# Kernel tuning notes

Hardware: AMD Instinct MI355X
Metric: run time of the kernel (lower is better)

The kernel has to match this reference:

```python
import jax, jax.numpy as jnp
import numpy as np

N = 50000
E = 800000
F_IN = 256
HID = 64
HEADS = 4
CLASSES = 8
NEG_SLOPE = 0.2  # PyG GATConv default


def setup_inputs() -> dict:
    key = jax.random.key(0)
    ks = jax.random.split(key, 10)
    x = jax.random.normal(ks[0], (N, F_IN), jnp.float32)
    edge_index = jax.random.randint(ks[1], (2, E), 0, N, dtype=jnp.int32)
    # layer 1: feature -> hidden, heads=4, concat
    W1 = jax.random.normal(ks[2], (F_IN, HEADS * HID), jnp.float32) / np.sqrt(F_IN).astype(np.float32)
    att1_src = jax.random.normal(ks[3], (HEADS, HID), jnp.float32) / np.sqrt(HID).astype(np.float32)
    att1_dst = jax.random.normal(ks[4], (HEADS, HID), jnp.float32) / np.sqrt(HID).astype(np.float32)
    b1 = jnp.zeros((HEADS * HID,), jnp.float32)
    # layer 2: hidden*heads -> classes, heads=1
    W2 = jax.random.normal(ks[5], (HEADS * HID, CLASSES), jnp.float32) / np.sqrt(HEADS * HID).astype(np.float32)
    att2_src = jax.random.normal(ks[6], (1, CLASSES), jnp.float32) / np.sqrt(CLASSES).astype(np.float32)
    att2_dst = jax.random.normal(ks[7], (1, CLASSES), jnp.float32) / np.sqrt(CLASSES).astype(np.float32)
    b2 = jnp.zeros((CLASSES,), jnp.float32)
    return {"x": x, "edge_index": edge_index, "W1": W1, "att1_src": att1_src,
            "att1_dst": att1_dst, "b1": b1, "W2": W2, "att2_src": att2_src,
            "att2_dst": att2_dst, "b2": b2}


def _gat_conv(x, W, a_src, a_dst, b, src, dst, heads, ch, n):
    # h: [N, H, C] per-head projected features
    h = (x @ W).reshape(n, heads, ch)
    alpha_src = jnp.einsum('nhc,hc->nh', h, a_src)  # [N, H]
    alpha_dst = jnp.einsum('nhc,hc->nh', h, a_dst)  # [N, H]
    # per-edge attention logits (gather along edges)
    e = jax.nn.leaky_relu(alpha_src[src] + alpha_dst[dst], NEG_SLOPE)  # [E, H]
    # segment softmax over edges sharing a destination node
    e_max = jax.ops.segment_max(e, dst, num_segments=n)  # [N, H]
    ex = jnp.exp(e - e_max[dst])
    denom = jax.ops.segment_sum(ex, dst, num_segments=n)  # [N, H]
    alpha = ex / denom[dst]  # self-loops guarantee denom > 0
    # weighted scatter-sum of source messages
    out = jax.ops.segment_sum(alpha[..., None] * h[src], dst, num_segments=n)  # [N, H, C]
    return out.reshape(n, heads * ch) + b


def reference(x, edge_index, W1, att1_src, att1_dst, b1, W2, att2_src, att2_dst, b2):
    n = x.shape[0]
    # PyG GATConv adds self-loops by default
    loop = jnp.arange(n, dtype=edge_index.dtype)
    src = jnp.concatenate([edge_index[0], loop])
    dst = jnp.concatenate([edge_index[1], loop])
    h = _gat_conv(x, W1, att1_src, att1_dst, b1, src, dst, HEADS, HID, n)
    h = jax.nn.relu(h)
    # dropout is identity in eval mode (training=self.training)
    out = _gat_conv(h, W2, att2_src, att2_dst, b2, src, dst, 1, CLASSES, n)
    return jax.nn.log_softmax(out, axis=1)
```

## Files before the change

kernel.cpp:

```cpp
#include <hip/hip_runtime.h>
#include <math.h>

#define NNODES 50000
#define NEDGES 800000
#define ETOT   850000
#define SLOPE  0.2f
#define BSLOTS 96
#define CPAD   16
#define NTILE  782
#define BBLK   518

typedef unsigned short ushort_t;
typedef unsigned int   uint_t;
typedef unsigned char  uchar_t;
typedef __attribute__((ext_vector_type(8))) __bf16 bf16x8;
typedef __attribute__((ext_vector_type(4))) float  floatx4;
typedef __attribute__((ext_vector_type(2))) float  floatx2;

#if defined(__has_builtin)
#if __has_builtin(__builtin_amdgcn_cvt_pk_f32_fp8) && __has_builtin(__builtin_amdgcn_cvt_pk_fp8_f32)
#define HWFP8 1
#endif
#endif

__device__ __forceinline__ float leaky(float v) { return fmaxf(v, SLOPE * v); }

__device__ __forceinline__ ushort_t f2bf(float f) {
    uint_t u = __float_as_uint(f);
    uint_t r = (u + 0x7fffu + ((u >> 16) & 1u)) >> 16;
    return (ushort_t)r;
}

__device__ __forceinline__ uint_t f2fp8_sw(float f) {
    uint_t u = __float_as_uint(f);
    uint_t s = (u >> 24) & 0x80u;
    u &= 0x7fffffffu;
    u = u + 0x7ffffu + ((u >> 20) & 1u);
    int e8 = (int)(u >> 23) - 120;
    uint_t m3 = (u >> 20) & 7u;
    if (e8 <= 0) return s;
    if (e8 >= 16) return s | 0x7eu;
    return s | ((uint_t)e8 << 3) | m3;
}
__device__ __forceinline__ float fp8tof_sw(uint_t b) {
    uint_t t = (b & 0x7fu) << 4;
    uint_t r = ((b & 0x80u) << 8) | (t + 0x3C00u);
    return (t >= 0x80u) ? __uint_as_float(r << 16) : 0.f;
}

__device__ __forceinline__ uint_t pk4fp8(float a, float b, float c, float d) {
#ifdef HWFP8
    int pk = 0;
    pk = __builtin_amdgcn_cvt_pk_fp8_f32(a, b, pk, false);
    pk = __builtin_amdgcn_cvt_pk_fp8_f32(c, d, pk, true);
    return (uint_t)pk;
#else
    return f2fp8_sw(a) | (f2fp8_sw(b) << 8) | (f2fp8_sw(c) << 16) | (f2fp8_sw(d) << 24);
#endif
}

__device__ __forceinline__ void dec8acc(uint2 v, float w, float* acc) {
#ifdef HWFP8
    floatx2 f0 = __builtin_amdgcn_cvt_pk_f32_fp8((int)v.x, false);
    floatx2 f1 = __builtin_amdgcn_cvt_pk_f32_fp8((int)v.x, true);
    floatx2 f2 = __builtin_amdgcn_cvt_pk_f32_fp8((int)v.y, false);
    floatx2 f3 = __builtin_amdgcn_cvt_pk_f32_fp8((int)v.y, true);
    acc[0] += w * f0.x; acc[1] += w * f0.y;
    acc[2] += w * f1.x; acc[3] += w * f1.y;
    acc[4] += w * f2.x; acc[5] += w * f2.y;
    acc[6] += w * f3.x; acc[7] += w * f3.y;
#else
    acc[0] += w * fp8tof_sw(v.x & 0xffu);
    acc[1] += w * fp8tof_sw((v.x >> 8) & 0xffu);
    acc[2] += w * fp8tof_sw((v.x >> 16) & 0xffu);
    acc[3] += w * fp8tof_sw(v.x >> 24);
    acc[4] += w * fp8tof_sw(v.y & 0xffu);
    acc[5] += w * fp8tof_sw((v.y >> 8) & 0xffu);
    acc[6] += w * fp8tof_sw((v.y >> 16) & 0xffu);
    acc[7] += w * fp8tof_sw(v.y >> 24);
#endif
}

__device__ __forceinline__ float hsel(float4 v, int h) {
    float t0 = (h & 1) ? v.y : v.x;
    float t1 = (h & 1) ? v.w : v.z;
    return (h & 2) ? t1 : t0;
}

__device__ __forceinline__ int esrc(const int* ei, int e) { return e < NEDGES ? ei[e]          : e - NEDGES; }
__device__ __forceinline__ int edst(const int* ei, int e) { return e < NEDGES ? ei[NEDGES + e] : e - NEDGES; }

__global__ void prep_k(const float* __restrict__ W1, ushort_t* __restrict__ W1c,
                       const float* __restrict__ b1, const float* __restrict__ W2,
                       float* __restrict__ b1p, float* __restrict__ W2p,
                       int* __restrict__ cnt) {
    int bid = blockIdx.x, tid = threadIdx.x;
    int gtid = bid * 256 + tid;
    if (bid < 256) {
        int k = gtid >> 8, n = gtid & 255;
        W1c[(k >> 5) * 8192 + n * 32 + (k & 31)] = f2bf(W1[gtid]);
    } else if (bid == 256) {
        int chp = tid;
        int q = chp & 63, cc = q >> 2, t = q & 3;
        int ch = (chp & 192) | (t * 16 + cc);
        b1p[chp] = b1[ch];
        #pragma unroll
        for (int j = 0; j < 8; ++j) W2p[chp * 8 + j] = W2[ch * 8 + j];
    }
    for (int i = gtid; i < NNODES * CPAD; i += 257 * 256) cnt[i] = 0;
}

__global__ __launch_bounds__(256) void gb_k(const float* __restrict__ X,
                                            const ushort_t* __restrict__ W1c,
                                            const float* __restrict__ att_s,
                                            const float* __restrict__ att_d,
                                            uchar_t* __restrict__ h1f,
                                            float* __restrict__ as1,
                                            float* __restrict__ ad1,
                                            const int* __restrict__ ei,
                                            int* __restrict__ cnt,
                                            int* __restrict__ bkt) {
    __shared__ ushort_t Als[64 * 40];
    __shared__ ushort_t Bls[256 * 40];
    int tid = threadIdx.x;

    if (blockIdx.x >= NTILE) {
        for (int e = (blockIdx.x - NTILE) * 256 + tid; e < ETOT; e += BBLK * 256) {
            int d = edst(ei, e), s = esrc(ei, e);
            int pos = atomicAdd(&cnt[d * CPAD], 1);
            if (pos < BSLOTS) bkt[d * BSLOTS + pos] = s;
        }
        return;
    }

    int row0 = blockIdx.x * 64;
    int wv = tid >> 6, lane = tid & 63, c15 = lane & 15, quad = lane >> 4;
    floatx4 acc[4][4] = {};

    for (int kc = 0; kc < 8; ++kc) {
        __syncthreads();
        {
            int r = tid >> 3, c4 = tid & 7;
            #pragma unroll
            for (int p = 0; p < 2; ++p) {
                int rr = r + p * 32;
                int row = row0 + rr;
                float4 v = make_float4(0.f, 0.f, 0.f, 0.f);
                if (row < NNODES) v = *(const float4*)&X[(size_t)row * 256 + kc * 32 + c4 * 4];
                uint2 pk;
                pk.x = (uint_t)f2bf(v.x) | ((uint_t)f2bf(v.y) << 16);
                pk.y = (uint_t)f2bf(v.z) | ((uint_t)f2bf(v.w) << 16);
                *(uint2*)&Als[rr * 40 + c4 * 4] = pk;
            }
        }
        {
            const uint4* srcp = (const uint4*)(W1c + kc * 8192);
            #pragma unroll
            for (int c = 0; c < 4; ++c) {
                int el = tid + c * 256;
                uint4 v = srcp[el];
                int n = el >> 2, kk8 = (el & 3) * 8;
                *(uint4*)&Bls[n * 40 + kk8] = v;
            }
        }
        __syncthreads();
        uint4 af[4], bfr[4];
        #pragma unroll
        for (int t = 0; t < 4; ++t)
            af[t] = *(const uint4*)&Als[(t * 16 + c15) * 40 + quad * 8];
        #pragma unroll
        for (int t = 0; t < 4; ++t)
            bfr[t] = *(const uint4*)&Bls[(wv * 64 + t * 16 + c15) * 40 + quad * 8];
        #pragma unroll
        for (int tm = 0; tm < 4; ++tm)
            #pragma unroll
            for (int tn = 0; tn < 4; ++tn)
                acc[tm][tn] = __builtin_amdgcn_mfma_f32_16x16x32_bf16(
                    __builtin_bit_cast(bf16x8, af[tm]),
                    __builtin_bit_cast(bf16x8, bfr[tn]),
                    acc[tm][tn], 0, 0, 0);
    }

    float asv[4], adv[4];
    #pragma unroll
    for (int tn = 0; tn < 4; ++tn) {
        asv[tn] = att_s[wv * 64 + tn * 16 + c15];
        adv[tn] = att_d[wv * 64 + tn * 16 + c15];
    }
    float ps[4][4], pd[4][4];
    #pragma unroll
    for (int tm = 0; tm < 4; ++tm)
        #pragma unroll
        for (int r = 0; r < 4; ++r) {
            float vs = 0.f, vd = 0.f;
            #pragma unroll
            for (int tn = 0; tn < 4; ++tn) {
                float a = acc[tm][tn][r];
                vs += a * asv[tn]; vd += a * adv[tn];
            }
            ps[tm][r] = vs; pd[tm][r] = vd;
        }
    #pragma unroll
    for (int tm = 0; tm < 4; ++tm) {
        #pragma unroll
        for (int r = 0; r < 4; ++r) {
            int row = row0 + tm * 16 + quad * 4 + r;
            if (row < NNODES) {
                uint_t pk = pk4fp8(acc[tm][0][r], acc[tm][1][r],
                                   acc[tm][2][r], acc[tm][3][r]);
                *(uint_t*)&h1f[(size_t)row * 256 + wv * 64 + c15 * 4] = pk;
            }
        }
    }
    #pragma unroll
    for (int off = 1; off < 16; off <<= 1)
        #pragma unroll
        for (int tm = 0; tm < 4; ++tm)
            #pragma unroll
            for (int r = 0; r < 4; ++r) {
                ps[tm][r] += __shfl_xor(ps[tm][r], off, 64);
                pd[tm][r] += __shfl_xor(pd[tm][r], off, 64);
            }
    if (c15 == 0) {
        #pragma unroll
        for (int tm = 0; tm < 4; ++tm)
            #pragma unroll
            for (int r = 0; r < 4; ++r) {
                int row = row0 + tm * 16 + quad * 4 + r;
                if (row < NNODES) {
                    as1[row * 4 + wv] = ps[tm][r];
                    ad1[row * 4 + wv] = pd[tm][r];
                }
            }
    }
}

#define PREL(BASE, VV)                                                          \
    {                                                                           \
        _Pragma("unroll")                                                       \
        for (int u = 0; u < 8; ++u) {                                           \
            int e = (BASE) + u;                                                 \
            int se = __shfl(s_reg, sbase + e, 64);                              \
            if (e < deg)                                                        \
                VV[u] = *(const uint2*)&h1f[(size_t)se * 256 + l32 * 8];        \
        }                                                                       \
    }
#define PREW(BASE, WW)                                                          \
    {                                                                           \
        _Pragma("unroll")                                                       \
        for (int u = 0; u < 8; ++u) WW[u] = wls[wv][half][(BASE) + u][h];       \
    }
#define CONS(BASE, VV, WW)                                                      \
    {                                                                           \
        _Pragma("unroll")                                                       \
        for (int u = 0; u < 8; ++u) {                                           \
            if ((BASE) + u < deg) dec8acc(VV[u], WW[u], acc);                   \
        }                                                                       \
    }

__global__ __launch_bounds__(256) void f1_k(const int* __restrict__ cnt,
                                            const int* __restrict__ bkt,
                                            const float* __restrict__ as1,
                                            const float* __restrict__ ad1,
                                            const uchar_t* __restrict__ h1f,
                                            const float* __restrict__ b1p,
                                            const float* __restrict__ W2p,
                                            const float* __restrict__ a2sw,
                                            const float* __restrict__ a2dw,
                                            float* __restrict__ h2,
                                            float* __restrict__ a2s,
                                            float* __restrict__ a2d) {
    int wv = threadIdx.x >> 6;
    int lane = threadIdx.x & 63;
    int half = lane >> 5, l32 = lane & 31;
    int node = blockIdx.x * 8 + wv * 2 + half;
    int h = l32 >> 3;
    int deg = min(cnt[node * CPAD], BSLOTS);
    const int* bp = bkt + (size_t)node * BSLOTS;
    float4 advec = *(const float4*)&ad1[(size_t)node * 4];
    __shared__ float wls[4][2][32][4];

    float acc[8] = {};
    float dn0, dn1, dn2, dn3;
    if (deg <= 32) {
        bool act = l32 < deg;
        int s_reg = node;
        if (act) s_reg = bp[l32];
        int sbase = half << 5;
        uint2 va[8], vb[8];
        float wa[8], wb[8];

        float4 av = *(const float4*)&as1[(size_t)s_reg * 4];
        PREL(0, va);
        if (deg > 8) PREL(8, vb);

        float e0 = act ? __expf(leaky(av.x + advec.x)) : 0.f;
        float e1 = act ? __expf(leaky(av.y + advec.y)) : 0.f;
        float e2 = act ? __expf(leaky(av.z + advec.z)) : 0.f;
        float e3 = act ? __expf(leaky(av.w + advec.w)) : 0.f;
        *(float4*)&wls[wv][half][l32][0] = make_float4(e0, e1, e2, e3);
        dn0 = e0; dn1 = e1; dn2 = e2; dn3 = e3;
        #pragma unroll
        for (int off = 16; off; off >>= 1) {
            dn0 += __shfl_xor(dn0, off, 64);
            dn1 += __shfl_xor(dn1, off, 64);
            dn2 += __shfl_xor(dn2, off, 64);
            dn3 += __shfl_xor(dn3, off, 64);
        }
        PREW(0, wa);
        if (deg > 8) PREW(8, wb);

        CONS(0, va, wa);
        if (deg > 8) {
            if (deg > 16) { PREL(16, va); PREW(16, wa); }
            CONS(8, vb, wb);
            if (deg > 16) {
                if (deg > 24) { PREL(24, vb); PREW(24, wb); }
                CONS(16, va, wa);
                if (deg > 24) CONS(24, vb, wb);
            }
        }
    } else {
        dn0 = dn1 = dn2 = dn3 = 0.f;
        for (int j = l32; j < deg; j += 32) {
            int s = bp[j];
            float4 av = *(const float4*)&as1[(size_t)s * 4];
            dn0 += __expf(leaky(av.x + advec.x));
            dn1 += __expf(leaky(av.y + advec.y));
            dn2 += __expf(leaky(av.z + advec.z));
            dn3 += __expf(leaky(av.w + advec.w));
        }
        #pragma unroll
        for (int off = 16; off; off >>= 1) {
            dn0 += __shfl_xor(dn0, off, 64);
            dn1 += __shfl_xor(dn1, off, 64);
            dn2 += __shfl_xor(dn2, off, 64);
            dn3 += __shfl_xor(dn3, off, 64);
        }
        float advh = hsel(advec, h);
        int cmax = deg - 1;
        for (int base = 0; base < deg; base += 8) {
            #pragma unroll
            for (int u = 0; u < 8; ++u) {
                int e = base + u;
                int ce = min(e, cmax);
                int se = bp[ce];
                float ash = as1[(size_t)se * 4 + h];
                float w = (e < deg) ? __expf(leaky(ash + advh)) : 0.f;
                uint2 v = *(const uint2*)&h1f[(size_t)se * 256 + l32 * 8];
                dec8acc(v, w, acc);
            }
        }
    }
    float rdh = 1.f / hsel(make_float4(dn0, dn1, dn2, dn3), h);
    #pragma unroll
    for (int c = 0; c < 8; ++c) acc[c] *= rdh;

    int k0 = l32 * 8;
    float4 ba = *(const float4*)&b1p[k0];
    float4 bb = *(const float4*)&b1p[k0 + 4];
    float xv[8];
    xv[0] = fmaxf(acc[0] + ba.x, 0.f); xv[1] = fmaxf(acc[1] + ba.y, 0.f);
    xv[2] = fmaxf(acc[2] + ba.z, 0.f); xv[3] = fmaxf(acc[3] + ba.w, 0.f);
    xv[4] = fmaxf(acc[4] + bb.x, 0.f); xv[5] = fmaxf(acc[5] + bb.y, 0.f);
    xv[6] = fmaxf(acc[6] + bb.z, 0.f); xv[7] = fmaxf(acc[7] + bb.w, 0.f);
    float p[8] = {};
    #pragma unroll
    for (int q = 0; q < 8; ++q) {
        const float4* w2p = (const float4*)&W2p[(size_t)(k0 + q) * 8];
        float4 wa2 = w2p[0], wb2 = w2p[1];
        p[0] += xv[q] * wa2.x; p[1] += xv[q] * wa2.y; p[2] += xv[q] * wa2.z; p[3] += xv[q] * wa2.w;
        p[4] += xv[q] * wb2.x; p[5] += xv[q] * wb2.y; p[6] += xv[q] * wb2.z; p[7] += xv[q] * wb2.w;
    }
    #pragma unroll
    for (int off = 16; off; off >>= 1)
        #pragma unroll
        for (int c = 0; c < 8; ++c) p[c] += __shfl_xor(p[c], off, 64);
    if (l32 == 0) {
        *(float4*)&h2[(size_t)node * 8]     = make_float4(p[0], p[1], p[2], p[3]);
        *(float4*)&h2[(size_t)node * 8 + 4] = make_float4(p[4], p[5], p[6], p[7]);
        float vs = 0.f, vd = 0.f;
        #pragma unroll
        for (int c = 0; c < 8; ++c) { vs += p[c] * a2sw[c]; vd += p[c] * a2dw[c]; }
        a2s[node] = vs; a2d[node] = vd;
    }
}

__global__ __launch_bounds__(256) void f2_k(const int* __restrict__ cnt,
                                            const int* __restrict__ bkt,
                                            const float* __restrict__ a2s,
                                            const float* __restrict__ a2d,
                                            const float* __restrict__ h2,
                                            const float* __restrict__ b2,
                                            float* __restrict__ out) {
    int wv = threadIdx.x >> 6;
    int lane = threadIdx.x & 63;
    int half = lane >> 5, l32 = lane & 31;
    int node = blockIdx.x * 8 + wv * 2 + half;
    int deg = min(cnt[node * CPAD], BSLOTS);
    const int* bp = bkt + (size_t)node * BSLOTS;
    float adv = a2d[node];

    float acc_a = 0.f, acc_b = 0.f;
    float den;
    int c = l32 & 7, eg = l32 >> 3;
    if (deg <= 32) {
        bool act = l32 < deg;
        int s_reg = node;
        if (act) s_reg = bp[l32];
        float ex = act ? __expf(leaky(a2s[s_reg] + adv)) : 0.f;
        den = ex;
        #pragma unroll
        for (int off = 16; off; off >>= 1) den += __shfl_xor(den, off, 64);
        int nb = (deg + 7) & ~7;
        int sbase = half << 5;
        for (int base = 0; base < nb; base += 8) {
            int e1 = base + eg, e2 = base + 4 + eg;
            int se1 = __shfl(s_reg, sbase + e1, 64);
            float w1 = __shfl(ex,    sbase + e1, 64);
            int se2 = __shfl(s_reg, sbase + e2, 64);
            float w2 = __shfl(ex,    sbase + e2, 64);
            acc_a += w1 * h2[(size_t)se1 * 8 + c];
            acc_b += w2 * h2[(size_t)se2 * 8 + c];
        }
    } else {
        den = 0.f;
        for (int j = l32; j < deg; j += 32) {
            int s = bp[j];
            den += __expf(leaky(a2s[s] + adv));
        }
        #pragma unroll
        for (int off = 16; off; off >>= 1) den += __shfl_xor(den, off, 64);
        int cmax = deg - 1;
        for (int base = 0; base < deg; base += 4) {
            int e = base + eg, ce = min(e, cmax);
            int se = bp[ce];
            float w = (e < deg) ? __expf(leaky(a2s[se] + adv)) : 0.f;
            acc_a += w * h2[(size_t)se * 8 + c];
        }
    }
    float acc = acc_a + acc_b;
    acc += __shfl_xor(acc, 8, 64);
    acc += __shfl_xor(acc, 16, 64);
    acc /= den;

    float v = acc + b2[c];
    float mx = v;
    #pragma unroll
    for (int off = 1; off < 8; off <<= 1) mx = fmaxf(mx, __shfl_xor(mx, off, 64));
    float ex2 = __expf(v - mx);
    float ss = ex2;
    #pragma unroll
    for (int off = 1; off < 8; off <<= 1) ss += __shfl_xor(ss, off, 64);
    if (l32 < 8) out[(size_t)node * 8 + c] = v - (mx + __logf(ss));
}

extern "C" void kernel_launch(void* const* d_in, const int* in_sizes, int n_in,
                              void* d_out, int out_size, void* d_ws, size_t ws_size,
                              hipStream_t stream) {
    const float* x    = (const float*)d_in[0];
    const int*   ei   = (const int*)  d_in[1];
    const float* W1   = (const float*)d_in[2];
    const float* a1sw = (const float*)d_in[3];
    const float* a1dw = (const float*)d_in[4];
    const float* b1   = (const float*)d_in[5];
    const float* W2   = (const float*)d_in[6];
    const float* a2sw = (const float*)d_in[7];
    const float* a2dw = (const float*)d_in[8];
    const float* b2   = (const float*)d_in[9];
    float* out = (float*)d_out;

    uchar_t* h1f = (uchar_t*)d_ws;
    ushort_t* W1c = (ushort_t*)(h1f + 12800000);
    float* as1  = (float*)(W1c + 65536);
    float* ad1  = as1 + 200000;
    float* h2   = ad1 + 200000;
    float* a2s  = h2  + 400000;
    float* a2d  = a2s + 50000;
    float* b1p  = a2d + 50000;
    float* W2p  = b1p + 256;
    int*   cnt  = (int*)(W2p + 2048);
    int*   bkt  = cnt + NNODES * CPAD;

    prep_k<<<257, 256, 0, stream>>>(W1, W1c, b1, W2, b1p, W2p, cnt);

    gb_k<<<NTILE + BBLK, 256, 0, stream>>>(x, W1c, a1sw, a1dw, h1f, as1, ad1,
                                           ei, cnt, bkt);

    f1_k<<<NNODES / 8, 256, 0, stream>>>(cnt, bkt, as1, ad1, h1f, b1p, W2p,
                                         a2sw, a2dw, h2, a2s, a2d);

    f2_k<<<NNODES / 8, 256, 0, stream>>>(cnt, bkt, a2s, a2d, h2, b2, out);
}
```

Baseline: 256.2 us.

## Hoist bucket loads and branch-free prefetch in GAT aggregation kernels

Both aggregation kernels now load the bucket slot unconditionally, alongside the degree and attention loads, so the dependent gathers are no longer serialised behind the count read. The branch decision uses the wave-wide max degree of the two half-wave nodes, which keeps the wave uniform. The f1 kernel drops per-edge bound checks: padded slots point at the node itself and carry weight 0, and feature gathers are issued before the exp and softmax reductions. The f2 kernel prefetches all h2 rows into registers before computing weights. This trades extra wasted gathers and more registers for memory-level parallelism, and it relies on bucket slots past deg being readable.

```diff
diff --git a/kernel.cpp b/kernel.cpp
--- a/kernel.cpp
+++ b/kernel.cpp
@@ -239,23 +239,15 @@
     {                                                                           \
         _Pragma("unroll")                                                       \
         for (int u = 0; u < 8; ++u) {                                           \
-            int e = (BASE) + u;                                                 \
-            int se = __shfl(s_reg, sbase + e, 64);                              \
-            if (e < deg)                                                        \
-                VV[u] = *(const uint2*)&h1f[(size_t)se * 256 + l32 * 8];        \
+            int se = __shfl(s_reg, sbase + (BASE) + u, 64);                     \
+            VV[u] = *(const uint2*)&h1f[(size_t)se * 256 + l32 * 8];            \
         }                                                                       \
     }
-#define PREW(BASE, WW)                                                          \
+#define CONS(BASE, VV)                                                          \
     {                                                                           \
         _Pragma("unroll")                                                       \
-        for (int u = 0; u < 8; ++u) WW[u] = wls[wv][half][(BASE) + u][h];       \
-    }
-#define CONS(BASE, VV, WW)                                                      \
-    {                                                                           \
-        _Pragma("unroll")                                                       \
-        for (int u = 0; u < 8; ++u) {                                           \
-            if ((BASE) + u < deg) dec8acc(VV[u], WW[u], acc);                   \
-        }                                                                       \
+        for (int u = 0; u < 8; ++u)                                             \
+            dec8acc(VV[u], wls[wv][half][(BASE) + u][h], acc);                  \
     }
 
 __global__ __launch_bounds__(256) void f1_k(const int* __restrict__ cnt,
@@ -275,30 +267,38 @@
     int half = lane >> 5, l32 = lane & 31;
     int node = blockIdx.x * 8 + wv * 2 + half;
     int h = l32 >> 3;
-    int deg = min(cnt[node * CPAD], BSLOTS);
-    const int* bp = bkt + (size_t)node * BSLOTS;
+    int sbase = half << 5;
+
+    int deg_raw = cnt[node * CPAD];
+    int bslot = bkt[(size_t)node * BSLOTS + l32];
     float4 advec = *(const float4*)&ad1[(size_t)node * 4];
+
+    int deg = min(deg_raw, BSLOTS);
+    int dm = max(deg, __shfl_xor(deg, 32, 64));
     __shared__ float wls[4][2][32][4];
 
     float acc[8] = {};
     float dn0, dn1, dn2, dn3;
-    if (deg <= 32) {
+    if (dm <= 32) {
         bool act = l32 < deg;
-        int s_reg = node;
-        if (act) s_reg = bp[l32];
-        int sbase = half << 5;
+        int s_reg = act ? bslot : node;
+        float4 av = *(const float4*)&as1[(size_t)s_reg * 4];
         uint2 va[8], vb[8];
-        float wa[8], wb[8];
-
-        float4 av = *(const float4*)&as1[(size_t)s_reg * 4];
         PREL(0, va);
-        if (deg > 8) PREL(8, vb);
+        PREL(8, vb);
 
         float e0 = act ? __expf(leaky(av.x + advec.x)) : 0.f;
         float e1 = act ? __expf(leaky(av.y + advec.y)) : 0.f;
         float e2 = act ? __expf(leaky(av.z + advec.z)) : 0.f;
         float e3 = act ? __expf(leaky(av.w + advec.w)) : 0.f;
         *(float4*)&wls[wv][half][l32][0] = make_float4(e0, e1, e2, e3);
+
+        int nb = (dm + 7) >> 3;
+        CONS(0, va);
+        if (nb > 2) PREL(16, va);
+        CONS(8, vb);
+        if (nb > 3) PREL(24, vb);
+
         dn0 = e0; dn1 = e1; dn2 = e2; dn3 = e3;
         #pragma unroll
         for (int off = 16; off; off >>= 1) {
@@ -307,20 +307,11 @@
             dn2 += __shfl_xor(dn2, off, 64);
             dn3 += __shfl_xor(dn3, off, 64);
         }
-        PREW(0, wa);
-        if (deg > 8) PREW(8, wb);
-
-        CONS(0, va, wa);
-        if (deg > 8) {
-            if (deg > 16) { PREL(16, va); PREW(16, wa); }
-            CONS(8, vb, wb);
-            if (deg > 16) {
-                if (deg > 24) { PREL(24, vb); PREW(24, wb); }
-                CONS(16, va, wa);
-                if (deg > 24) CONS(24, vb, wb);
-            }
-        }
+
+        if (nb > 2) CONS(16, va);
+        if (nb > 3) CONS(24, vb);
     } else {
+        const int* bp = bkt + (size_t)node * BSLOTS;
         dn0 = dn1 = dn2 = dn3 = 0.f;
         for (int j = l32; j < deg; j += 32) {
             int s = bp[j];
@@ -397,33 +388,51 @@
     int lane = threadIdx.x & 63;
     int half = lane >> 5, l32 = lane & 31;
     int node = blockIdx.x * 8 + wv * 2 + half;
-    int deg = min(cnt[node * CPAD], BSLOTS);
-    const int* bp = bkt + (size_t)node * BSLOTS;
+    int sbase = half << 5;
+
+    int deg_raw = cnt[node * CPAD];
+    int bslot = bkt[(size_t)node * BSLOTS + l32];
     float adv = a2d[node];
+
+    int deg = min(deg_raw, BSLOTS);
+    int dm = max(deg, __shfl_xor(deg, 32, 64));
 
     float acc_a = 0.f, acc_b = 0.f;
     float den;
     int c = l32 & 7, eg = l32 >> 3;
-    if (deg <= 32) {
+    if (dm <= 32) {
         bool act = l32 < deg;
-        int s_reg = node;
-        if (act) s_reg = bp[l32];
-        float ex = act ? __expf(leaky(a2s[s_reg] + adv)) : 0.f;
+        int s_reg = act ? bslot : node;
+        float asv = a2s[(size_t)s_reg];
+        int nb = (dm + 7) >> 3;
+
+        float hv1[4], hv2[4];
+        #pragma unroll
+        for (int p2 = 0; p2 < 4; ++p2) {
+            if (p2 < nb) {
+                int se1 = __shfl(s_reg, sbase + p2 * 8 + eg, 64);
+                int se2 = __shfl(s_reg, sbase + p2 * 8 + 4 + eg, 64);
+                hv1[p2] = h2[(size_t)se1 * 8 + c];
+                hv2[p2] = h2[(size_t)se2 * 8 + c];
+            }
+        }
+
+        float ex = act ? __expf(leaky(asv + adv)) : 0.f;
         den = ex;
         #pragma unroll
         for (int off = 16; off; off >>= 1) den += __shfl_xor(den, off, 64);
-        int nb = (deg + 7) & ~7;
-        int sbase = half << 5;
-        for (int base = 0; base < nb; base += 8) {
-            int e1 = base + eg, e2 = base + 4 + eg;
-            int se1 = __shfl(s_reg, sbase + e1, 64);
-            float w1 = __shfl(ex,    sbase + e1, 64);
-            int se2 = __shfl(s_reg, sbase + e2, 64);
-            float w2 = __shfl(ex,    sbase + e2, 64);
-            acc_a += w1 * h2[(size_t)se1 * 8 + c];
-            acc_b += w2 * h2[(size_t)se2 * 8 + c];
+
+        #pragma unroll
+        for (int p2 = 0; p2 < 4; ++p2) {
+            if (p2 < nb) {
+                float w1 = __shfl(ex, sbase + p2 * 8 + eg, 64);
+                float w2 = __shfl(ex, sbase + p2 * 8 + 4 + eg, 64);
+                acc_a += w1 * hv1[p2];
+                acc_b += w2 * hv2[p2];
+            }
         }
     } else {
+        const int* bp = bkt + (size_t)node * BSLOTS;
         den = 0.f;
         for (int j = l32; j < deg; j += 32) {
             int s = bp[j];
```

Result: slower. 264.9 us (+3.4%).

## Gather 16-byte fp8 feature chunks with two edges per half-wave in layer-1 aggregation

Applied to the files above, without the earlier changes.

Each half-wave now splits its 32 lanes into two groups of 16. Each lane loads 16 fp8 features (a uint4) instead of 8, and the two groups process alternate edges in parallel. Partial accumulators are combined with a cross-group shuffle before normalisation and the fused W2 projection. This halves the number of gather instructions and edge iterations per node, at the cost of twice the accumulator registers and an extra reduction step.

```diff
diff --git a/kernel.cpp b/kernel.cpp
--- a/kernel.cpp
+++ b/kernel.cpp
@@ -59,25 +59,26 @@
 #endif
 }
 
-__device__ __forceinline__ void dec8acc(uint2 v, float w, float* acc) {
+__device__ __forceinline__ void dec16acc(uint4 v, float w, float* acc) {
 #ifdef HWFP8
-    floatx2 f0 = __builtin_amdgcn_cvt_pk_f32_fp8((int)v.x, false);
-    floatx2 f1 = __builtin_amdgcn_cvt_pk_f32_fp8((int)v.x, true);
-    floatx2 f2 = __builtin_amdgcn_cvt_pk_f32_fp8((int)v.y, false);
-    floatx2 f3 = __builtin_amdgcn_cvt_pk_f32_fp8((int)v.y, true);
-    acc[0] += w * f0.x; acc[1] += w * f0.y;
-    acc[2] += w * f1.x; acc[3] += w * f1.y;
-    acc[4] += w * f2.x; acc[5] += w * f2.y;
-    acc[6] += w * f3.x; acc[7] += w * f3.y;
+    floatx2 f;
+    f = __builtin_amdgcn_cvt_pk_f32_fp8((int)v.x, false); acc[0]  += w * f.x; acc[1]  += w * f.y;
+    f = __builtin_amdgcn_cvt_pk_f32_fp8((int)v.x, true);  acc[2]  += w * f.x; acc[3]  += w * f.y;
+    f = __builtin_amdgcn_cvt_pk_f32_fp8((int)v.y, false); acc[4]  += w * f.x; acc[5]  += w * f.y;
+    f = __builtin_amdgcn_cvt_pk_f32_fp8((int)v.y, true);  acc[6]  += w * f.x; acc[7]  += w * f.y;
+    f = __builtin_amdgcn_cvt_pk_f32_fp8((int)v.z, false); acc[8]  += w * f.x; acc[9]  += w * f.y;
+    f = __builtin_amdgcn_cvt_pk_f32_fp8((int)v.z, true);  acc[10] += w * f.x; acc[11] += w * f.y;
+    f = __builtin_amdgcn_cvt_pk_f32_fp8((int)v.w, false); acc[12] += w * f.x; acc[13] += w * f.y;
+    f = __builtin_amdgcn_cvt_pk_f32_fp8((int)v.w, true);  acc[14] += w * f.x; acc[15] += w * f.y;
 #else
-    acc[0] += w * fp8tof_sw(v.x & 0xffu);
-    acc[1] += w * fp8tof_sw((v.x >> 8) & 0xffu);
-    acc[2] += w * fp8tof_sw((v.x >> 16) & 0xffu);
-    acc[3] += w * fp8tof_sw(v.x >> 24);
-    acc[4] += w * fp8tof_sw(v.y & 0xffu);
-    acc[5] += w * fp8tof_sw((v.y >> 8) & 0xffu);
-    acc[6] += w * fp8tof_sw((v.y >> 16) & 0xffu);
-    acc[7] += w * fp8tof_sw(v.y >> 24);
+    uint_t ws[4] = {v.x, v.y, v.z, v.w};
+    #pragma unroll
+    for (int q = 0; q < 4; ++q) {
+        acc[q*4+0] += w * fp8tof_sw(ws[q] & 0xffu);
+        acc[q*4+1] += w * fp8tof_sw((ws[q] >> 8) & 0xffu);
+        acc[q*4+2] += w * fp8tof_sw((ws[q] >> 16) & 0xffu);
+        acc[q*4+3] += w * fp8tof_sw(ws[q] >> 24);
+    }
 #endif
 }
 
@@ -238,23 +239,23 @@
 #define PREL(BASE, VV)                                                          \
     {                                                                           \
         _Pragma("unroll")                                                       \
-        for (int u = 0; u < 8; ++u) {                                           \
-            int e = (BASE) + u;                                                 \
+        for (int j = 0; j < 4; ++j) {                                           \
+            int e = (BASE) + 2 * j + g;                                         \
             int se = __shfl(s_reg, sbase + e, 64);                              \
             if (e < deg)                                                        \
-                VV[u] = *(const uint2*)&h1f[(size_t)se * 256 + l32 * 8];        \
+                VV[j] = *(const uint4*)&h1f[(size_t)se * 256 + koff];           \
         }                                                                       \
     }
 #define PREW(BASE, WW)                                                          \
     {                                                                           \
         _Pragma("unroll")                                                       \
-        for (int u = 0; u < 8; ++u) WW[u] = wls[wv][half][(BASE) + u][h];       \
+        for (int j = 0; j < 4; ++j) WW[j] = wls[wv][half][(BASE) + 2*j + g][h]; \
     }
 #define CONS(BASE, VV, WW)                                                      \
     {                                                                           \
         _Pragma("unroll")                                                       \
-        for (int u = 0; u < 8; ++u) {                                           \
-            if ((BASE) + u < deg) dec8acc(VV[u], WW[u], acc);                   \
+        for (int j = 0; j < 4; ++j) {                                           \
+            if ((BASE) + 2 * j + g < deg) dec16acc(VV[j], WW[j], acc);          \
         }                                                                       \
     }
 
@@ -274,21 +275,23 @@
     int lane = threadIdx.x & 63;
     int half = lane >> 5, l32 = lane & 31;
     int node = blockIdx.x * 8 + wv * 2 + half;
-    int h = l32 >> 3;
+    int g = l32 >> 4;
+    int koff = (l32 & 15) * 16;
+    int h = (l32 & 15) >> 2;
     int deg = min(cnt[node * CPAD], BSLOTS);
     const int* bp = bkt + (size_t)node * BSLOTS;
     float4 advec = *(const float4*)&ad1[(size_t)node * 4];
     __shared__ float wls[4][2][32][4];
 
-    float acc[8] = {};
+    float acc[16] = {};
     float dn0, dn1, dn2, dn3;
     if (deg <= 32) {
         bool act = l32 < deg;
         int s_reg = node;
         if (act) s_reg = bp[l32];
         int sbase = half << 5;
-        uint2 va[8], vb[8];
-        float wa[8], wb[8];
+        uint4 va[4], vb[4];
+        float wa[4], wb[4];
 
         float4 av = *(const float4*)&as1[(size_t)s_reg * 4];
         PREL(0, va);
@@ -339,41 +342,43 @@
         }
         float advh = hsel(advec, h);
         int cmax = deg - 1;
-        for (int base = 0; base < deg; base += 8) {
-            #pragma unroll
-            for (int u = 0; u < 8; ++u) {
-                int e = base + u;
-                int ce = min(e, cmax);
-                int se = bp[ce];
-                float ash = as1[(size_t)se * 4 + h];
-                float w = (e < deg) ? __expf(leaky(ash + advh)) : 0.f;
-                uint2 v = *(const uint2*)&h1f[(size_t)se * 256 + l32 * 8];
-                dec8acc(v, w, acc);
-            }
+        for (int base = 0; base < deg; base += 2) {
+            int e = base + g;
+            int ce = min(e, cmax);
+            int se = bp[ce];
+            float ash = as1[(size_t)se * 4 + h];
+            float w = (e < deg) ? __expf(leaky(ash + advh)) : 0.f;
+            uint4 v = *(const uint4*)&h1f[(size_t)se * 256 + koff];
+            dec16acc(v, w, acc);
         }
     }
     float rdh = 1.f / hsel(make_float4(dn0, dn1, dn2, dn3), h);
     #pragma unroll
-    for (int c = 0; c < 8; ++c) acc[c] *= rdh;
-
-    int k0 = l32 * 8;
-    float4 ba = *(const float4*)&b1p[k0];
-    float4 bb = *(const float4*)&b1p[k0 + 4];
-    float xv[8];
-    xv[0] = fmaxf(acc[0] + ba.x, 0.f); xv[1] = fmaxf(acc[1] + ba.y, 0.f);
-    xv[2] = fmaxf(acc[2] + ba.z, 0.f); xv[3] = fmaxf(acc[3] + ba.w, 0.f);
-    xv[4] = fmaxf(acc[4] + bb.x, 0.f); xv[5] = fmaxf(acc[5] + bb.y, 0.f);
-    xv[6] = fmaxf(acc[6] + bb.z, 0.f); xv[7] = fmaxf(acc[7] + bb.w, 0.f);
+    for (int c = 0; c < 16; ++c) {
+        acc[c] += __shfl_xor(acc[c], 16, 64);
+        acc[c] *= rdh;
+    }
+
+    int k0 = (l32 & 15) * 16;
+    float xv[16];
+    #pragma unroll
+    for (int q4 = 0; q4 < 4; ++q4) {
+        float4 bq = *(const float4*)&b1p[k0 + q4 * 4];
+        xv[q4*4+0] = fmaxf(acc[q4*4+0] + bq.x, 0.f);
+        xv[q4*4+1] = fmaxf(acc[q4*4+1] + bq.y, 0.f);
+        xv[q4*4+2] = fmaxf(acc[q4*4+2] + bq.z, 0.f);
+        xv[q4*4+3] = fmaxf(acc[q4*4+3] + bq.w, 0.f);
+    }
     float p[8] = {};
     #pragma unroll
-    for (int q = 0; q < 8; ++q) {
+    for (int q = 0; q < 16; ++q) {
         const float4* w2p = (const float4*)&W2p[(size_t)(k0 + q) * 8];
         float4 wa2 = w2p[0], wb2 = w2p[1];
         p[0] += xv[q] * wa2.x; p[1] += xv[q] * wa2.y; p[2] += xv[q] * wa2.z; p[3] += xv[q] * wa2.w;
         p[4] += xv[q] * wb2.x; p[5] += xv[q] * wb2.y; p[6] += xv[q] * wb2.z; p[7] += xv[q] * wb2.w;
     }
     #pragma unroll
-    for (int off = 16; off; off >>= 1)
+    for (int off = 8; off; off >>= 1)
         #pragma unroll
         for (int c = 0; c < 8; ++c) p[c] += __shfl_xor(p[c], off, 64);
     if (l32 == 0) {
```

Measured after the change: 304.9 us. 1.19x slower.

## Read W1 fragments from global directly and prefetch next X chunk into registers

Applied to the files above, without the earlier changes.

Drops the shared-memory staging buffer for the bf16 W1 tile, so each wave loads its B fragments straight from global/L2. It also software-pipelines the X tile: the next k-chunk's float4 values are fetched into registers while the current chunk's MFMAs run. This removes one barrier's worth of LDS traffic and cuts LDS usage, which may raise occupancy. In exchange, W1 loads now go through uncoalesced-ish 16-byte global reads on every k-step in every block, and register pressure rises.

```diff
diff --git a/kernel.cpp b/kernel.cpp
--- a/kernel.cpp
+++ b/kernel.cpp
@@ -121,7 +121,6 @@
                                             int* __restrict__ cnt,
                                             int* __restrict__ bkt) {
     __shared__ ushort_t Als[64 * 40];
-    __shared__ ushort_t Bls[256 * 40];
     int tid = threadIdx.x;
 
     if (blockIdx.x >= NTILE) {
@@ -137,40 +136,38 @@
     int wv = tid >> 6, lane = tid & 63, c15 = lane & 15, quad = lane >> 4;
     floatx4 acc[4][4] = {};
 
+    int r = tid >> 3, c4 = tid & 7;
+    int rowA = row0 + r, rowB = row0 + r + 32;
+    float4 pa0 = make_float4(0.f, 0.f, 0.f, 0.f);
+    float4 pa1 = make_float4(0.f, 0.f, 0.f, 0.f);
+    if (rowA < NNODES) pa0 = *(const float4*)&X[(size_t)rowA * 256 + c4 * 4];
+    if (rowB < NNODES) pa1 = *(const float4*)&X[(size_t)rowB * 256 + c4 * 4];
+
     for (int kc = 0; kc < 8; ++kc) {
+        if (kc) __syncthreads();
+        {
+            uint2 pk;
+            pk.x = (uint_t)f2bf(pa0.x) | ((uint_t)f2bf(pa0.y) << 16);
+            pk.y = (uint_t)f2bf(pa0.z) | ((uint_t)f2bf(pa0.w) << 16);
+            *(uint2*)&Als[r * 40 + c4 * 4] = pk;
+            pk.x = (uint_t)f2bf(pa1.x) | ((uint_t)f2bf(pa1.y) << 16);
+            pk.y = (uint_t)f2bf(pa1.z) | ((uint_t)f2bf(pa1.w) << 16);
+            *(uint2*)&Als[(r + 32) * 40 + c4 * 4] = pk;
+        }
         __syncthreads();
-        {
-            int r = tid >> 3, c4 = tid & 7;
-            #pragma unroll
-            for (int p = 0; p < 2; ++p) {
-                int rr = r + p * 32;
-                int row = row0 + rr;
-                float4 v = make_float4(0.f, 0.f, 0.f, 0.f);
-                if (row < NNODES) v = *(const float4*)&X[(size_t)row * 256 + kc * 32 + c4 * 4];
-                uint2 pk;
-                pk.x = (uint_t)f2bf(v.x) | ((uint_t)f2bf(v.y) << 16);
-                pk.y = (uint_t)f2bf(v.z) | ((uint_t)f2bf(v.w) << 16);
-                *(uint2*)&Als[rr * 40 + c4 * 4] = pk;
-            }
-        }
-        {
-            const uint4* srcp = (const uint4*)(W1c + kc * 8192);
-            #pragma unroll
-            for (int c = 0; c < 4; ++c) {
-                int el = tid + c * 256;
-                uint4 v = srcp[el];
-                int n = el >> 2, kk8 = (el & 3) * 8;
-                *(uint4*)&Bls[n * 40 + kk8] = v;
-            }
-        }
-        __syncthreads();
+        if (kc < 7) {
+            pa0 = make_float4(0.f, 0.f, 0.f, 0.f);
+            pa1 = make_float4(0.f, 0.f, 0.f, 0.f);
+            if (rowA < NNODES) pa0 = *(const float4*)&X[(size_t)rowA * 256 + (kc + 1) * 32 + c4 * 4];
+            if (rowB < NNODES) pa1 = *(const float4*)&X[(size_t)rowB * 256 + (kc + 1) * 32 + c4 * 4];
+        }
         uint4 af[4], bfr[4];
         #pragma unroll
         for (int t = 0; t < 4; ++t)
             af[t] = *(const uint4*)&Als[(t * 16 + c15) * 40 + quad * 8];
         #pragma unroll
         for (int t = 0; t < 4; ++t)
-            bfr[t] = *(const uint4*)&Bls[(wv * 64 + t * 16 + c15) * 40 + quad * 8];
+            bfr[t] = *(const uint4*)&W1c[kc * 8192 + (wv * 64 + t * 16 + c15) * 32 + quad * 8];
         #pragma unroll
         for (int tm = 0; tm < 4; ++tm)
             #pragma unroll
@@ -191,23 +188,23 @@
     #pragma unroll
     for (int tm = 0; tm < 4; ++tm)
         #pragma unroll
-        for (int r = 0; r < 4; ++r) {
+        for (int r2 = 0; r2 < 4; ++r2) {
             float vs = 0.f, vd = 0.f;
             #pragma unroll
             for (int tn = 0; tn < 4; ++tn) {
-                float a = acc[tm][tn][r];
+                float a = acc[tm][tn][r2];
                 vs += a * asv[tn]; vd += a * adv[tn];
             }
-            ps[tm][r] = vs; pd[tm][r] = vd;
+            ps[tm][r2] = vs; pd[tm][r2] = vd;
         }
     #pragma unroll
     for (int tm = 0; tm < 4; ++tm) {
         #pragma unroll
-        for (int r = 0; r < 4; ++r) {
-            int row = row0 + tm * 16 + quad * 4 + r;
+        for (int r2 = 0; r2 < 4; ++r2) {
+            int row = row0 + tm * 16 + quad * 4 + r2;
             if (row < NNODES) {
-                uint_t pk = pk4fp8(acc[tm][0][r], acc[tm][1][r],
-                                   acc[tm][2][r], acc[tm][3][r]);
+                uint_t pk = pk4fp8(acc[tm][0][r2], acc[tm][1][r2],
+                                   acc[tm][2][r2], acc[tm][3][r2]);
                 *(uint_t*)&h1f[(size_t)row * 256 + wv * 64 + c15 * 4] = pk;
             }
         }
@@ -217,19 +214,19 @@
         #pragma unroll
         for (int tm = 0; tm < 4; ++tm)
             #pragma unroll
-            for (int r = 0; r < 4; ++r) {
-                ps[tm][r] += __shfl_xor(ps[tm][r], off, 64);
-                pd[tm][r] += __shfl_xor(pd[tm][r], off, 64);
+            for (int r2 = 0; r2 < 4; ++r2) {
+                ps[tm][r2] += __shfl_xor(ps[tm][r2], off, 64);
+                pd[tm][r2] += __shfl_xor(pd[tm][r2], off, 64);
             }
     if (c15 == 0) {
         #pragma unroll
         for (int tm = 0; tm < 4; ++tm)
             #pragma unroll
-            for (int r = 0; r < 4; ++r) {
-                int row = row0 + tm * 16 + quad * 4 + r;
+            for (int r2 = 0; r2 < 4; ++r2) {
+                int row = row0 + tm * 16 + quad * 4 + r2;
                 if (row < NNODES) {
-                    as1[row * 4 + wv] = ps[tm][r];
-                    ad1[row * 4 + wv] = pd[tm][r];
+                    as1[row * 4 + wv] = ps[tm][r2];
+                    ad1[row * 4 + wv] = pd[tm][r2];
                 }
             }
     }
```

Result: no change. 254.1 us (-0.8%).
